# Kernel tuning notes

Measured on AMD Instinct MI355X. Metric: run time of the kernel, lower is better.

## Reference

```python
import jax, jax.numpy as jnp
import numpy as np

K = 3            # snake kernel size
MORPH = 0        # extend along depth axis
EXT = 1.0        # extend_scope
EPS = 1e-5
GROUPS = 16      # out_planes // 4


def conv3d(x, w, b, stride=(1, 1, 1), padding='SAME'):
    out = jax.lax.conv_general_dilated(
        x, w, window_strides=stride, padding=padding,
        dimension_numbers=('NCDHW', 'OIDHW', 'NCDHW'))
    return out + b[None, :, None, None, None]


def batchnorm(x, g, b):
    # training-mode BatchNorm3d (batch statistics, biased variance)
    m = x.mean(axis=(0, 2, 3, 4), keepdims=True)
    v = x.var(axis=(0, 2, 3, 4), keepdims=True)
    return (x - m) / jnp.sqrt(v + EPS) * g[None, :, None, None, None] + b[None, :, None, None, None]


def groupnorm(x, g, b):
    B, C, D, H, W = x.shape
    xg = x.reshape(B, GROUPS, C // GROUPS, D, H, W)
    m = xg.mean(axis=(2, 3, 4, 5), keepdims=True)
    v = xg.var(axis=(2, 3, 4, 5), keepdims=True)
    xn = ((xg - m) / jnp.sqrt(v + EPS)).reshape(B, C, D, H, W)
    return xn * g[None, :, None, None, None] + b[None, :, None, None, None]


def cumulative_offsets(off):
    # off: [B, K, D, H, W]; accumulate outward from kernel center (snake chaining)
    center = K // 2
    cums = [None] * K
    cums[center] = jnp.zeros_like(off[:, 0])
    for i in range(1, center + 1):
        cums[center + i] = cums[center + i - 1] + off[:, center + i]
        cums[center - i] = cums[center - i + 1] + off[:, center - i]
    return jnp.stack(cums, axis=1)  # [B, K, D, H, W]


def trilinear_sample_one(feat, z, y, x):
    # feat: [C, D, H, W]; z/y/x: [DK, H, W] float coords (already clamped)
    C, D, H, W = feat.shape
    z0f, y0f, x0f = jnp.floor(z), jnp.floor(y), jnp.floor(x)
    wz, wy, wx = z - z0f, y - y0f, x - x0f
    z0 = jnp.clip(z0f.astype(jnp.int32), 0, D - 1)
    y0 = jnp.clip(y0f.astype(jnp.int32), 0, H - 1)
    x0 = jnp.clip(x0f.astype(jnp.int32), 0, W - 1)
    z1 = jnp.clip(z0 + 1, 0, D - 1)
    y1 = jnp.clip(y0 + 1, 0, H - 1)
    x1 = jnp.clip(x0 + 1, 0, W - 1)

    def g(zi, yi, xi):
        return feat[:, zi, yi, xi]  # [C, DK, H, W]

    out = (g(z0, y0, x0) * ((1 - wz) * (1 - wy) * (1 - wx))[None]
         + g(z0, y0, x1) * ((1 - wz) * (1 - wy) * wx)[None]
         + g(z0, y1, x0) * ((1 - wz) * wy * (1 - wx))[None]
         + g(z0, y1, x1) * ((1 - wz) * wy * wx)[None]
         + g(z1, y0, x0) * (wz * (1 - wy) * (1 - wx))[None]
         + g(z1, y0, x1) * (wz * (1 - wy) * wx)[None]
         + g(z1, y1, x0) * (wz * wy * (1 - wx))[None]
         + g(z1, y1, x1) * (wz * wy * wx)[None])
    return out


def setup_inputs() -> dict:
    key = jax.random.key(0)
    ks = jax.random.split(key, 8)
    B, Cin, Cout, D, H, W = 2, 32, 64, 48, 48, 48
    x = jax.random.normal(ks[0], (B, Cin, D, H, W), dtype=jnp.float32)
    offset_w = jax.random.normal(ks[1], (3 * K, Cin, 3, 3, 3), dtype=jnp.float32) * 0.02
    offset_b = jnp.zeros((3 * K,), dtype=jnp.float32)
    bn_g = jnp.ones((3 * K,), dtype=jnp.float32)
    bn_b = jnp.zeros((3 * K,), dtype=jnp.float32)
    conv_w = jax.random.normal(ks[2], (Cout, Cin, K, 1, 1), dtype=jnp.float32) * 0.05
    conv_b = jnp.zeros((Cout,), dtype=jnp.float32)
    gn_g = jnp.ones((Cout,), dtype=jnp.float32)
    gn_b = jnp.zeros((Cout,), dtype=jnp.float32)
    return {"x": x, "offset_w": offset_w, "offset_b": offset_b, "bn_g": bn_g,
            "bn_b": bn_b, "conv_w": conv_w, "conv_b": conv_b, "gn_g": gn_g, "gn_b": gn_b}


def reference(x, offset_w, offset_b, bn_g, bn_b, conv_w, conv_b, gn_g, gn_b):
    B, C, D, H, W = x.shape
    dt = x.dtype
    # offset prediction: tanh(BN(conv3x3x3)) -> [B, 3K, D, H, W]
    off = jnp.tanh(batchnorm(conv3d(x, offset_w, offset_b), bn_g, bn_b))
    off_y = off[:, K:2 * K]   # perpendicular offsets (morph=0: H and W)
    off_x = off[:, 2 * K:]
    cy = cumulative_offsets(off_y)  # [B, K, D, H, W]
    cx = cumulative_offsets(off_x)
    center = K // 2
    kk = jnp.arange(K, dtype=dt) - center
    # coordinate maps [B, K, D, H, W]
    z = jnp.broadcast_to(jnp.arange(D, dtype=dt)[None, None, :, None, None]
                         + kk[None, :, None, None, None], (B, K, D, H, W))
    y = jnp.arange(H, dtype=dt)[None, None, None, :, None] + EXT * cy
    xc = jnp.arange(W, dtype=dt)[None, None, None, None, :] + EXT * cx
    z = jnp.clip(z, 0.0, D - 1)
    y = jnp.clip(y, 0.0, H - 1)
    xc = jnp.clip(xc, 0.0, W - 1)
    # interleave kernel points along depth: [B, D*K, H, W]
    il = lambda c: jnp.transpose(c, (0, 2, 1, 3, 4)).reshape(B, D * K, H, W)
    z, y, xc = il(z), il(y), il(xc)
    deformed = jax.vmap(trilinear_sample_one)(x, z, y, xc)  # [B, C, D*K, H, W]
    out = conv3d(deformed, conv_w, conv_b, stride=(K, 1, 1), padding='VALID')
    return jax.nn.relu(groupnorm(out, gn_g, gn_b))
```

## Files before the change

kernel.cpp:

```cpp
#include <hip/hip_runtime.h>
#include <hip/hip_bf16.h>

#define ZB    2
#define ZCIN  32
#define ZCOUT 64
#define ZD    48
#define ZH    48
#define ZW    48
#define ZHW   2304
#define ZDHW  110592
#define ZNPOS 221184
#define ZEPS  1e-5f

#define WFLAG    0
#define WCB      64
#define WBNSTAT  128
#define WGNSTAT  192
#define WBMAT    256
#define WBMATO   3328
#define WCONV    10240
#define WXTP     894976


template <int TAG>
__device__ __forceinline__ float ldT(const void* p, long i) {
    if (TAG == 1) return __bfloat162float(((const __hip_bfloat16*)p)[i]);
    return ((const float*)p)[i];
}

__device__ __forceinline__ unsigned short f2bu(float f) {
    unsigned int b = __float_as_uint(f);
    b += 0x7FFFu + ((b >> 16) & 1u);
    return (unsigned short)(b >> 16);
}
__device__ __forceinline__ float bu2f(unsigned short u) {
    return __uint_as_float(((unsigned int)u) << 16);
}

typedef short bf16x8 __attribute__((ext_vector_type(8)));
typedef float f32x4  __attribute__((ext_vector_type(4)));
typedef unsigned short u16x8 __attribute__((ext_vector_type(8)));

template <int TAG>
__device__ void begin_prep(const void* offset_w, const void* conv_w,
                           const void* conv_b, float* ws, int i) {
    if (i < 64) {
        ws[WCB + i] = ldT<TAG>(conv_b, i);
    } else if (i < 6208) {
        int j = i - 64;
        int n = j / 96, kk = j % 96;
        int kz = kk >> 5, ci = kk & 31;
        ((unsigned short*)(ws + WBMAT))[j] =
            f2bu(ldT<TAG>(conv_w, ((long)n * 32 + ci) * 3 + kz));
    } else if (i < 20032) {
        int j = i - 6208;
        int tap = j / 512, rem = j % 512;
        int n = rem >> 5, ci = rem & 31;
        float v = 0.f;
        if (n < 4) {
            int ch = (n == 0) ? 3 : (n == 1) ? 5 : (n == 2) ? 6 : 8;
            v = ldT<TAG>(offset_w, (long)ch * 864 + ci * 27 + tap);
        }
        ((unsigned short*)(ws + WBMATO))[j] = f2bu(v);
    } else if (i < 20160) {
        ws[WBNSTAT + (i - 20032)] = 0.0f;
    }
}

__device__ void begin_zero_boundary(float* ws, int v) {
    if (v >= 28816) return;
    int b = v / 14408, r = v % 14408;
    int z, y, x;
    if (r < 5000) {
        z = (r / 2500) * 49; int q = r % 2500; y = q / 50; x = q % 50;
    } else if (r < 9800) {
        int s = r - 5000; z = 1 + s / 100; int q = s % 100;
        y = (q / 50) * 49; x = q % 50;
    } else {
        int s = r - 9800; z = 1 + s / 96; int q = s % 96;
        y = 1 + q / 2; x = (q & 1) * 49;
    }
    unsigned short* xtp = (unsigned short*)(ws + WXTP);
    long base = ((((long)b * 50 + z) * 50 + y) * 50 + x) * 32;
    u16x8 zz = {0, 0, 0, 0, 0, 0, 0, 0};
#pragma unroll
    for (int k = 0; k < 4; ++k) *(u16x8*)&xtp[base + k * 8] = zz;
}

template <int TAG>
__device__ void begin_xpose(const void* x, float* ws, int bid2,
                            unsigned short* tile) {
    int b = bid2 / 2304, rem = bid2 % 2304;
    int z = rem / 48, y = rem % 48;
    int t = threadIdx.x;
    long ibase = (long)b * ZCIN * ZDHW + (long)z * ZHW + (long)y * ZW;
#pragma unroll
    for (int k = 0; k < 6; ++k) {
        int e = k * 256 + t;
        int ci = e / 48, xx = e % 48;
        tile[xx * 34 + ci] = f2bu(ldT<TAG>(x, ibase + (long)ci * ZDHW + xx));
    }
    __syncthreads();
    long obase16 = ((((long)b * 50 + z + 1) * 50 + y + 1) * 50 + 1) * 32;
    unsigned int* o32 = (unsigned int*)((unsigned short*)(ws + WXTP) + obase16);
#pragma unroll
    for (int k = 0; k < 3; ++k) {
        int e2 = k * 256 + t;
        int xx = e2 >> 4, c2 = (e2 & 15) * 2;
        o32[e2] = (unsigned int)tile[xx * 34 + c2]
                | ((unsigned int)tile[xx * 34 + c2 + 1] << 16);
    }
}

__global__ void __launch_bounds__(256) zk_begin(const void* x, const void* offset_w,
                                                const void* conv_w, const void* conv_b,
                                                const unsigned short* bng, float* ws) {
    __shared__ unsigned short tile[48 * 34];
    int bid = blockIdx.x;
    bool isbf = (bng[0] != 0);
    if (bid < 79) {
        int i = bid * 256 + threadIdx.x;
        if (i == 0) ws[WFLAG] = isbf ? 1.0f : 2.0f;
        if (isbf) begin_prep<1>(offset_w, conv_w, conv_b, ws, i);
        else      begin_prep<2>(offset_w, conv_w, conv_b, ws, i);
    } else if (bid < 192) {
        begin_zero_boundary(ws, (bid - 79) * 256 + threadIdx.x);
    } else {
        if (isbf) begin_xpose<1>(x, ws, bid - 192, tile);
        else      begin_xpose<2>(x, ws, bid - 192, tile);
    }
}

__global__ void __launch_bounds__(256, 3) zk_offset_conv(float* ws) {
    const unsigned short* bmo = (const unsigned short*)(ws + WBMATO);
    const unsigned short* xtp = (const unsigned short*)(ws + WXTP);
    float* convout = ws + WCONV;

    __shared__ float sred[8];

    int t = threadIdx.x, lane = t & 63, wv = t >> 6;
    int quad = lane >> 4, col = lane & 15;
    int bid2 = (blockIdx.x & 7) * 216 + (blockIdx.x >> 3);

    if (t < 8) sred[t] = 0.f;

    long abase[2];
#pragma unroll
    for (int mt = 0; mt < 2; ++mt) {
        int p = bid2 * 128 + wv * 32 + mt * 16 + col;
        int b = p / ZDHW; int r = p - b * ZDHW;
        int z = r / ZHW;  int r2 = r - z * ZHW;
        int y = r2 / 48;  int x = r2 - y * 48;
        abase[mt] = ((((long)(b * 50 + z + 1) * 50) + y + 1) * 50 + x + 1) * 32
                    + quad * 8;
    }

    f32x4 acc0 = {0.f, 0.f, 0.f, 0.f};
    f32x4 acc1 = {0.f, 0.f, 0.f, 0.f};

    __syncthreads();

#pragma unroll
    for (int kz = 0; kz < 3; ++kz) {
        bf16x8 bfr[9], a0[9], a1[9];
#pragma unroll
        for (int j = 0; j < 9; ++j) {
            int ky = j / 3, kx = j % 3;
            long off = ((long)(kz - 1) * 2500 + (ky - 1) * 50 + (kx - 1)) * 32;
            a0[j]  = *(const bf16x8*)&xtp[abase[0] + off];
            a1[j]  = *(const bf16x8*)&xtp[abase[1] + off];
            bfr[j] = *(const bf16x8*)&bmo[((kz * 9 + j) * 16 + col) * 32 + quad * 8];
        }
#pragma unroll
        for (int j = 0; j < 9; ++j) {
            acc0 = __builtin_amdgcn_mfma_f32_16x16x32_bf16(a0[j], bfr[j], acc0, 0, 0, 0);
            acc1 = __builtin_amdgcn_mfma_f32_16x16x32_bf16(a1[j], bfr[j], acc1, 0, 0, 0);
        }
    }

    float S = acc0[0] + acc0[1] + acc0[2] + acc0[3]
            + acc1[0] + acc1[1] + acc1[2] + acc1[3];
    float Q = acc0[0] * acc0[0] + acc0[1] * acc0[1] + acc0[2] * acc0[2] + acc0[3] * acc0[3]
            + acc1[0] * acc1[0] + acc1[1] * acc1[1] + acc1[2] * acc1[2] + acc1[3] * acc1[3];
    S += __shfl_xor(S, 16); S += __shfl_xor(S, 32);
    Q += __shfl_xor(Q, 16); Q += __shfl_xor(Q, 32);

    if (col < 4) {
        int pbase = bid2 * 128 + wv * 32 + quad * 4;
        *(f32x4*)&convout[col * ZNPOS + pbase]      = acc0;
        *(f32x4*)&convout[col * ZNPOS + pbase + 16] = acc1;
        if (quad == 0) {
            atomicAdd(&sred[col], S);
            atomicAdd(&sred[4 + col], Q);
        }
    }
    __syncthreads();
    if (t < 8) atomicAdd(&ws[WBNSTAT + t], sred[t]);
}

__device__ __forceinline__ void sample_plane(const unsigned short* xt,
        unsigned short* As, int tp, int kzslot, int b, int zp, int h, int w,
        float cy, float cx) {
    float fy = fminf(fmaxf((float)h + cy, 0.f), 47.f);
    float fx = fminf(fmaxf((float)w + cx, 0.f), 47.f);
    int y0 = (int)fy, x0 = (int)fx;
    float wy = fy - (float)y0, wx = fx - (float)x0;
    int y1 = (y0 < 47) ? y0 + 1 : 47, x1 = (x0 < 47) ? x0 + 1 : 47;
    long pb = ((long)b * 50 + zp + 1) * 50;
    long r0 = (pb + y0 + 1) * 50, r1 = (pb + y1 + 1) * 50;
    long a00 = (r0 + x0 + 1) * 32, a01 = (r0 + x1 + 1) * 32;
    long a10 = (r1 + x0 + 1) * 32, a11 = (r1 + x1 + 1) * 32;
    float u00 = (1.f - wy) * (1.f - wx), u01 = (1.f - wy) * wx;
    float u10 = wy * (1.f - wx),         u11 = wy * wx;
    u16x8 A[4], B[4], C[4], D[4];
#pragma unroll
    for (int j = 0; j < 4; ++j) {
        A[j] = *(const u16x8*)&xt[a00 + j * 8];
        B[j] = *(const u16x8*)&xt[a01 + j * 8];
        C[j] = *(const u16x8*)&xt[a10 + j * 8];
        D[j] = *(const u16x8*)&xt[a11 + j * 8];
    }
#pragma unroll
    for (int j = 0; j < 4; ++j) {
        u16x8 o;
#pragma unroll
        for (int e = 0; e < 8; ++e) {
            float v = u00 * bu2f((unsigned short)A[j][e])
                    + u01 * bu2f((unsigned short)B[j][e])
                    + u10 * bu2f((unsigned short)C[j][e])
                    + u11 * bu2f((unsigned short)D[j][e]);
            o[e] = f2bu(v);
        }
        *(u16x8*)&As[tp * 104 + kzslot * 32 + j * 8] = o;
    }
}

template <int TAG>
__device__ void deform_body(const void* bn_g, const void* bn_b,
                            float* ws, void* out,
                            unsigned short* As, float* sred) {
    const float* cb  = ws + WCB;
    const float* cvo = ws + WCONV;
    const unsigned short* bm = (const unsigned short*)(ws + WBMAT);
    const unsigned short* xt = (const unsigned short*)(ws + WXTP);
    float* gnstat = ws + WGNSTAT;

    int t    = threadIdx.x;
    int tp   = t & 255;
    int half = t >> 8;
    int bid  = blockIdx.x;
    int slab = (bid & 7) * 108 + (bid >> 3);
    int p    = slab * 256 + tp;
    int b    = p / ZDHW;
    int r    = p - b * ZDHW;
    int d = r / ZHW, r2 = r % ZHW;
    int h = r2 / ZW, w = r2 % ZW;

    if (t < 32) sred[t] = 0.f;

    float bnsc[4], bnsh[4];
#pragma unroll
    for (int c = 0; c < 4; ++c) {
        int ch = (c == 0) ? 3 : (c == 1) ? 5 : (c == 2) ? 6 : 8;
        float sum = ws[WBNSTAT + c], sq = ws[WBNSTAT + 4 + c];
        float mean = sum / (float)ZNPOS;
        float var  = sq / (float)ZNPOS - mean * mean;
        float inv  = rsqrtf(var + ZEPS);
        float g = ldT<TAG>(bn_g, ch), bb = ldT<TAG>(bn_b, ch);
        bnsc[c] = inv * g;
        bnsh[c] = bb - mean * inv * g;
    }

    if (half == 0) {
        float cy = tanhf(fmaf(cvo[p],             bnsc[0], bnsh[0]));
        float cx = tanhf(fmaf(cvo[2 * ZNPOS + p], bnsc[2], bnsh[2]));
        int zp = (d > 0) ? d - 1 : 0;
        sample_plane(xt, As, tp, 0, b, zp, h, w, cy, cx);
    } else {
        long base1 = ((((long)b * 50 + d + 1) * 50 + h + 1) * 50 + (w + 1)) * 32;
#pragma unroll
        for (int j = 0; j < 4; ++j)
            *(u16x8*)&As[tp * 104 + 32 + j * 8] = *(const u16x8*)&xt[base1 + j * 8];
        float cy = tanhf(fmaf(cvo[ZNPOS + p],     bnsc[1], bnsh[1]));
        float cx = tanhf(fmaf(cvo[3 * ZNPOS + p], bnsc[3], bnsh[3]));
        int zp = (d < ZD - 1) ? d + 1 : ZD - 1;
        sample_plane(xt, As, tp, 2, b, zp, h, w, cy, cx);
    }
    __syncthreads();

    int lane = t & 63, wv = t >> 6;
    int quad = lane >> 4, col = lane & 15;
    f32x4 acc[2][4];
#pragma unroll
    for (int nt = 0; nt < 4; ++nt) {
        float bias = cb[nt * 16 + col];
#pragma unroll
        for (int mt = 0; mt < 2; ++mt) {
            acc[mt][nt][0] = bias; acc[mt][nt][1] = bias;
            acc[mt][nt][2] = bias; acc[mt][nt][3] = bias;
        }
    }
#pragma unroll
    for (int kz = 0; kz < 3; ++kz) {
        bf16x8 bfr[4];
#pragma unroll
        for (int nt = 0; nt < 4; ++nt)
            bfr[nt] = *(const bf16x8*)&bm[(nt * 16 + col) * 96 + kz * 32 + quad * 8];
#pragma unroll
        for (int mt = 0; mt < 2; ++mt) {
            bf16x8 afr = *(const bf16x8*)&As[(32 * wv + 16 * mt + col) * 104
                                             + kz * 32 + quad * 8];
#pragma unroll
            for (int nt = 0; nt < 4; ++nt)
                acc[mt][nt] = __builtin_amdgcn_mfma_f32_16x16x32_bf16(
                                  afr, bfr[nt], acc[mt][nt], 0, 0, 0);
        }
    }

    int r0 = r - tp;
    long obase = (long)b * ZCOUT * ZDHW;
#pragma unroll
    for (int nt = 0; nt < 4; ++nt) {
        int co = nt * 16 + col;
        float S = 0.f, Q = 0.f;
        long cobase = obase + (long)co * ZDHW;
#pragma unroll
        for (int mt = 0; mt < 2; ++mt) {
            long rbase = cobase + r0 + 32 * wv + 16 * mt + quad * 4;
            f32x4 v = acc[mt][nt];
            S += v[0] + v[1] + v[2] + v[3];
            Q += v[0] * v[0] + v[1] * v[1] + v[2] * v[2] + v[3] * v[3];
            if (TAG == 2) {
                *(f32x4*)((float*)out + rbase) = v;
            } else {
                unsigned int lo = (unsigned int)f2bu(v[0]) | ((unsigned int)f2bu(v[1]) << 16);
                unsigned int hi = (unsigned int)f2bu(v[2]) | ((unsigned int)f2bu(v[3]) << 16);
                uint2 pk; pk.x = lo; pk.y = hi;
                *(uint2*)((__hip_bfloat16*)out + rbase) = pk;
            }
        }
        S += __shfl_xor(S, 16); S += __shfl_xor(S, 32);
        Q += __shfl_xor(Q, 16); Q += __shfl_xor(Q, 32);
        if (quad == 0) {
            int g = nt * 4 + (col >> 2);
            atomicAdd(&sred[g], S);
            atomicAdd(&sred[16 + g], Q);
        }
    }
    __syncthreads();
    if (t < 32) {
        int g = t & 15, isq = t >> 4;
        atomicAdd(&gnstat[isq * 32 + b * 16 + g], sred[t]);
    }
}

__global__ void __launch_bounds__(512, 4) zk_deform(const void* bn_g, const void* bn_b,
                                                    float* ws, void* out) {
    __shared__ __align__(16) unsigned short As[256 * 104];
    __shared__ float sred[32];
    if (ws[WFLAG] == 1.0f) deform_body<1>(bn_g, bn_b, ws, out, As, sred);
    else                   deform_body<2>(bn_g, bn_b, ws, out, As, sred);
}

template <int TAG>
__device__ void gn_body(void* out, const float* ws, const void* gn_g, const void* gn_b) {
    long i0 = ((long)blockIdx.x * 256 + threadIdx.x) * 8;
    int bc = (int)(i0 / ZDHW);
    int b = bc >> 6, co = bc & 63, g = co >> 2;
    float sum = ws[WGNSTAT + b * 16 + g];
    float sq  = ws[WGNSTAT + 32 + b * 16 + g];
    const float N = 4.0f * (float)ZDHW;
    float mean = sum / N;
    float var  = sq / N - mean * mean;
    float inv  = rsqrtf(var + ZEPS);
    float gg = ldT<TAG>(gn_g, co), gb = ldT<TAG>(gn_b, co);
    float scale = inv * gg;
    float shift = gb - mean * inv * gg;

    if (TAG == 1) {
        u16x8* vp = (u16x8*)((__hip_bfloat16*)out + i0);
        u16x8 v = *vp;
#pragma unroll
        for (int j = 0; j < 8; ++j) {
            float f = bu2f((unsigned short)v[j]);
            f = fmaxf(fmaf(f, scale, shift), 0.f);
            v[j] = f2bu(f);
        }
        *vp = v;
    } else {
        float4* op = (float4*)((float*)out + i0);
        float4 v0 = op[0], v1 = op[1];
        v0.x = fmaxf(fmaf(v0.x, scale, shift), 0.f);
        v0.y = fmaxf(fmaf(v0.y, scale, shift), 0.f);
        v0.z = fmaxf(fmaf(v0.z, scale, shift), 0.f);
        v0.w = fmaxf(fmaf(v0.w, scale, shift), 0.f);
        v1.x = fmaxf(fmaf(v1.x, scale, shift), 0.f);
        v1.y = fmaxf(fmaf(v1.y, scale, shift), 0.f);
        v1.z = fmaxf(fmaf(v1.z, scale, shift), 0.f);
        v1.w = fmaxf(fmaf(v1.w, scale, shift), 0.f);
        op[0] = v0; op[1] = v1;
    }
}

__global__ void __launch_bounds__(256) zk_gn_apply(void* out, const float* ws,
                                                   const void* gn_g, const void* gn_b) {
    if (ws[WFLAG] == 1.0f) gn_body<1>(out, ws, gn_g, gn_b);
    else                   gn_body<2>(out, ws, gn_g, gn_b);
}

extern "C" void kernel_launch(void* const* d_in, const int* in_sizes, int n_in,
                              void* d_out, int out_size, void* d_ws, size_t ws_size,
                              hipStream_t stream) {
    const void* x        = d_in[0];
    const void* offset_w = d_in[1];
    const void* bn_g     = d_in[3];
    const void* bn_b     = d_in[4];
    const void* conv_w   = d_in[5];
    const void* conv_b   = d_in[6];
    const void* gn_g     = d_in[7];
    const void* gn_b     = d_in[8];
    float* ws = (float*)d_ws;

    zk_begin<<<4800, 256, 0, stream>>>(x, offset_w, conv_w, conv_b,
                                       (const unsigned short*)bn_g, ws);

    zk_offset_conv<<<1728, 256, 0, stream>>>(ws);

    zk_deform<<<864, 512, 0, stream>>>(bn_g, bn_b, ws, d_out);

    int ngn = out_size / 8 / 256;
    zk_gn_apply<<<ngn, 256, 0, stream>>>(d_out, ws, gn_g, gn_b);
}
```

Before: 187.3 us.

## Stage padded input slices in LDS for offset conv and vectorize transpose loads

The offset conv kernel now copies a 6x50-position halo slice per depth tap into shared memory and reads all 27 tap operands from LDS. Each block covers four full rows (three 16-wide M tiles per wave) instead of scattered 128 positions, and the grid changes to match. This cuts redundant global loads of overlapping neighborhoods at the cost of extra LDS traffic and syncs. The input transpose also switches to 16-byte vector loads instead of per-element scalar loads.

Result: faster. 173.5 us (-7.4%).

```diff
diff --git a/kernel.cpp b/kernel.cpp
--- a/kernel.cpp
+++ b/kernel.cpp
@@ -94,11 +94,29 @@
     int z = rem / 48, y = rem % 48;
     int t = threadIdx.x;
     long ibase = (long)b * ZCIN * ZDHW + (long)z * ZHW + (long)y * ZW;
-#pragma unroll
-    for (int k = 0; k < 6; ++k) {
-        int e = k * 256 + t;
-        int ci = e / 48, xx = e % 48;
-        tile[xx * 34 + ci] = f2bu(ldT<TAG>(x, ibase + (long)ci * ZDHW + xx));
+    if (TAG == 1) {
+        if (t < 192) {
+            int ci = t / 6, cb = t % 6;
+            u16x8 v = *(const u16x8*)((const unsigned short*)x
+                                      + ibase + (long)ci * ZDHW + cb * 8);
+#pragma unroll
+            for (int e = 0; e < 8; ++e)
+                tile[(cb * 8 + e) * 34 + ci] = (unsigned short)v[e];
+        }
+    } else {
+#pragma unroll
+        for (int kk = 0; kk < 2; ++kk) {
+            int c = t + kk * 256;
+            if (c < 384) {
+                int ci = c / 12, cb = c % 12;
+                float4 v = *(const float4*)((const float*)x
+                                            + ibase + (long)ci * ZDHW + cb * 4);
+                tile[(cb * 4 + 0) * 34 + ci] = f2bu(v.x);
+                tile[(cb * 4 + 1) * 34 + ci] = f2bu(v.y);
+                tile[(cb * 4 + 2) * 34 + ci] = f2bu(v.z);
+                tile[(cb * 4 + 3) * 34 + ci] = f2bu(v.w);
+            }
+        }
     }
     __syncthreads();
     long obase16 = ((((long)b * 50 + z + 1) * 50 + y + 1) * 50 + 1) * 32;
@@ -131,64 +149,75 @@
     }
 }
 
-__global__ void __launch_bounds__(256, 3) zk_offset_conv(float* ws) {
+__global__ void __launch_bounds__(256, 4) zk_offset_conv(float* ws) {
     const unsigned short* bmo = (const unsigned short*)(ws + WBMATO);
     const unsigned short* xtp = (const unsigned short*)(ws + WXTP);
     float* convout = ws + WCONV;
 
+    __shared__ __align__(16) unsigned short slice[1280 * 8];
     __shared__ float sred[8];
 
     int t = threadIdx.x, lane = t & 63, wv = t >> 6;
     int quad = lane >> 4, col = lane & 15;
-    int bid2 = (blockIdx.x & 7) * 216 + (blockIdx.x >> 3);
+    int bid2 = (blockIdx.x & 7) * 144 + (blockIdx.x >> 3);
+    int b  = bid2 / 576, rem = bid2 % 576;
+    int z  = rem / 12, yt = rem % 12;
+    int y0 = yt * 4;
 
     if (t < 8) sred[t] = 0.f;
 
-    long abase[2];
-#pragma unroll
-    for (int mt = 0; mt < 2; ++mt) {
-        int p = bid2 * 128 + wv * 32 + mt * 16 + col;
-        int b = p / ZDHW; int r = p - b * ZDHW;
-        int z = r / ZHW;  int r2 = r - z * ZHW;
-        int y = r2 / 48;  int x = r2 - y * 48;
-        abase[mt] = ((((long)(b * 50 + z + 1) * 50) + y + 1) * 50 + x + 1) * 32
-                    + quad * 8;
-    }
-
-    f32x4 acc0 = {0.f, 0.f, 0.f, 0.f};
-    f32x4 acc1 = {0.f, 0.f, 0.f, 0.f};
-
-    __syncthreads();
+    f32x4 acc[3];
+#pragma unroll
+    for (int mt = 0; mt < 3; ++mt) {
+        acc[mt][0] = 0.f; acc[mt][1] = 0.f; acc[mt][2] = 0.f; acc[mt][3] = 0.f;
+    }
 
 #pragma unroll
     for (int kz = 0; kz < 3; ++kz) {
-        bf16x8 bfr[9], a0[9], a1[9];
-#pragma unroll
-        for (int j = 0; j < 9; ++j) {
-            int ky = j / 3, kx = j % 3;
-            long off = ((long)(kz - 1) * 2500 + (ky - 1) * 50 + (kx - 1)) * 32;
-            a0[j]  = *(const bf16x8*)&xtp[abase[0] + off];
-            a1[j]  = *(const bf16x8*)&xtp[abase[1] + off];
+        long cb = (((long)b * 50 + (z + kz)) * 50 + y0) * 50 * 4;
+        __syncthreads();
+#pragma unroll
+        for (int i = 0; i < 5; ++i) {
+            int c = i * 256 + t;
+            *(u16x8*)&slice[c * 8] = *(const u16x8*)&xtp[(cb + c) * 8];
+        }
+        __syncthreads();
+
+        bf16x8 bfr[9];
+#pragma unroll
+        for (int j = 0; j < 9; ++j)
             bfr[j] = *(const bf16x8*)&bmo[((kz * 9 + j) * 16 + col) * 32 + quad * 8];
-        }
-#pragma unroll
-        for (int j = 0; j < 9; ++j) {
-            acc0 = __builtin_amdgcn_mfma_f32_16x16x32_bf16(a0[j], bfr[j], acc0, 0, 0, 0);
-            acc1 = __builtin_amdgcn_mfma_f32_16x16x32_bf16(a1[j], bfr[j], acc1, 0, 0, 0);
-        }
-    }
-
-    float S = acc0[0] + acc0[1] + acc0[2] + acc0[3]
-            + acc1[0] + acc1[1] + acc1[2] + acc1[3];
-    float Q = acc0[0] * acc0[0] + acc0[1] * acc0[1] + acc0[2] * acc0[2] + acc0[3] * acc0[3]
-            + acc1[0] * acc1[0] + acc1[1] * acc1[1] + acc1[2] * acc1[2] + acc1[3] * acc1[3];
+
+#pragma unroll
+        for (int ky = 0; ky < 3; ++ky)
+#pragma unroll
+            for (int kx = 0; kx < 3; ++kx) {
+                int j = ky * 3 + kx;
+#pragma unroll
+                for (int mt = 0; mt < 3; ++mt) {
+                    int ch = ((wv + ky) * 50 + mt * 16 + col + kx) * 4 + quad;
+                    bf16x8 a = *(const bf16x8*)&slice[ch * 8];
+                    acc[mt] = __builtin_amdgcn_mfma_f32_16x16x32_bf16(
+                                  a, bfr[j], acc[mt], 0, 0, 0);
+                }
+            }
+    }
+
+    float S = 0.f, Q = 0.f;
+#pragma unroll
+    for (int mt = 0; mt < 3; ++mt) {
+        S += acc[mt][0] + acc[mt][1] + acc[mt][2] + acc[mt][3];
+        Q += acc[mt][0] * acc[mt][0] + acc[mt][1] * acc[mt][1]
+           + acc[mt][2] * acc[mt][2] + acc[mt][3] * acc[mt][3];
+    }
     S += __shfl_xor(S, 16); S += __shfl_xor(S, 32);
     Q += __shfl_xor(Q, 16); Q += __shfl_xor(Q, 32);
 
     if (col < 4) {
-        int pbase = bid2 * 128 + wv * 32 + quad * 4;
-        *(f32x4*)&convout[col * ZNPOS + pbase]      = acc0;
-        *(f32x4*)&convout[col * ZNPOS + pbase + 16] = acc1;
+        int rowbase = b * ZDHW + z * ZHW + (y0 + wv) * 48 + quad * 4;
+#pragma unroll
+        for (int mt = 0; mt < 3; ++mt)
+            *(f32x4*)&convout[col * ZNPOS + rowbase + mt * 16] = acc[mt];
         if (quad == 0) {
             atomicAdd(&sred[col], S);
             atomicAdd(&sred[4 + col], Q);
@@ -424,7 +453,7 @@
     zk_begin<<<4800, 256, 0, stream>>>(x, offset_w, conv_w, conv_b,
                                        (const unsigned short*)bn_g, ws);
 
-    zk_offset_conv<<<1728, 256, 0, stream>>>(ws);
+    zk_offset_conv<<<1152, 256, 0, stream>>>(ws);
 
     zk_deform<<<864, 512, 0, stream>>>(bn_g, bn_b, ws, d_out);
 
```
